# Kernel optimization log

Measured on AMD Instinct MI355X. Metric: run time of the kernel, lower is better.

The kernel has to match this reference:

```python
import jax, jax.numpy as jnp
import numpy as np

BETA = 0.25

def setup_inputs() -> dict:
    key = jax.random.key(0)
    k1, k2 = jax.random.split(key)
    N, K, D = 32768, 8192, 512
    latents = jax.random.normal(k1, (N, D), dtype=jnp.float32)
    # torch init: uniform(-1/num_protos, 1/num_protos)
    prototypes = jax.random.uniform(k2, (K, D), dtype=jnp.float32, minval=-1.0 / K, maxval=1.0 / K)
    return {"latents": latents, "prototypes": prototypes}


def reference(latents, prototypes):
    dists = (jnp.sum(latents ** 2, axis=1, keepdims=True)
             + jnp.sum(prototypes ** 2, axis=1)
             - 2.0 * jnp.matmul(latents, prototypes.T))
    closest = jnp.argmin(dists, axis=1)  # [N]
    # one-hot @ prototypes == gather (same math, no NxK intermediate)
    quantized = prototypes[closest]  # [N, D]
    commitment_loss = jnp.mean((jax.lax.stop_gradient(quantized) - latents) ** 2)
    embedding_loss = jnp.mean((quantized - jax.lax.stop_gradient(latents)) ** 2)
    vq_loss = commitment_loss * BETA + embedding_loss
    # straight-through estimator
    quantized_st = latents + jax.lax.stop_gradient(quantized - latents)
    return quantized_st, vq_loss
```

## Files before the change

### kernel.cpp

```cpp
#include <hip/hip_runtime.h>


#define N_ROWS 32768
#define K_PROTO 8192
#define DIM 512
#define BM 256
#define BN 128
#define BKB 128
#define GROUPS 8
#define TILES 8
#define NSTEP 32
#define BUFB 16384

typedef unsigned char u8;
typedef unsigned int u32;
typedef __attribute__((ext_vector_type(4))) int i32x4;
typedef __attribute__((ext_vector_type(8))) int i32x8;
typedef __attribute__((ext_vector_type(4))) float f32x4;

__device__ __forceinline__ void async16(const void* g, void* s) {
    __builtin_amdgcn_global_load_lds(
        (const __attribute__((address_space(1))) void*)g,
        (__attribute__((address_space(3))) void*)s, 16, 0, 0);
}

__device__ __forceinline__ int pk4(float a, float b, float c, float d) {
    int v = 0;
    v = __builtin_amdgcn_cvt_pk_fp8_f32(a, b, v, false);
    v = __builtin_amdgcn_cvt_pk_fp8_f32(c, d, v, true);
    return v;
}

__global__ void __launch_bounds__(256) conv_latents(const float* __restrict__ X,
                                                    u8* __restrict__ Xf,
                                                    u32* __restrict__ best) {
    if (blockIdx.x < 128) best[blockIdx.x * 256 + threadIdx.x] = 0xFFFFFFFFu;
    size_t i = ((size_t)blockIdx.x * 256 + threadIdx.x) * 16;
    float4 a = ((const float4*)(X + i))[0];
    float4 b = ((const float4*)(X + i))[1];
    float4 c = ((const float4*)(X + i))[2];
    float4 d = ((const float4*)(X + i))[3];
    int4 o;
    o.x = pk4(a.x, a.y, a.z, a.w);
    o.y = pk4(b.x, b.y, b.z, b.w);
    o.z = pk4(c.x, c.y, c.z, c.w);
    o.w = pk4(d.x, d.y, d.z, d.w);
    *(int4*)(Xf + i) = o;
}

__global__ void __launch_bounds__(256) conv_protos(const float* __restrict__ P,
                                                   u8* __restrict__ Pf,
                                                   float* __restrict__ pnC) {
    int row  = blockIdx.x * 4 + (threadIdx.x >> 6);
    int lane = threadIdx.x & 63;
    const float* src = P + (size_t)row * DIM + lane * 8;
    float4 a = ((const float4*)src)[0];
    float4 b = ((const float4*)src)[1];
    int2 o;
    o.x = pk4(a.x * 8192.0f, a.y * 8192.0f, a.z * 8192.0f, a.w * 8192.0f);
    o.y = pk4(b.x * 8192.0f, b.y * 8192.0f, b.z * 8192.0f, b.w * 8192.0f);
    *(int2*)(Pf + (size_t)row * DIM + lane * 8) = o;
    float ss = a.x*a.x + a.y*a.y + a.z*a.z + a.w*a.w
             + b.x*b.x + b.y*b.y + b.z*b.z + b.w*b.w;
    #pragma unroll
    for (int off = 32; off; off >>= 1) ss += __shfl_down(ss, off);
    if (lane == 0) pnC[row] = ss * 8192.0f + 256.0f;
}

__device__ __forceinline__ void stage_b(const u8* __restrict__ Pf, u8* BsF,
                                        int s2, int colg, const int (&voff)[4],
                                        int tid) {
    const int t2 = s2 >> 2, kt2 = s2 & 3, sb = s2 % 3;
    const u8* src = Pf + (size_t)(colg + t2 * BN) * DIM + kt2 * BKB;
    u8* dst = BsF + sb * BUFB + tid * 16;
    #pragma unroll
    for (int i = 0; i < 4; i++)
        async16(src + voff[i], dst + i * 4096);
}

__global__ void __launch_bounds__(256, 1) vq_score_kernel(const u8* __restrict__ Xf,
                                                          const u8* __restrict__ Pf,
                                                          const float* __restrict__ pnC,
                                                          u32* __restrict__ best) {
    __shared__ __align__(16) u8 lds_raw[3 * BUFB + 8192];
    u8* BsF = lds_raw;
    const float* pcs = (const float*)(lds_raw + 3 * BUFB);

    const int tid  = threadIdx.x;
    const int row0 = blockIdx.x * BM;
    const int colg = blockIdx.y * (TILES * BN);

    const int w    = tid >> 6, lane = tid & 63;
    const int quad = lane >> 4, l15 = lane & 15;

    int voff[4];
    #pragma unroll
    for (int i = 0; i < 4; i++) {
        int f = tid + i * 256;
        int row = f >> 3, c = (f & 7) ^ (row & 7);
        voff[i] = row * DIM + c * 16;
    }

    const int x7   = l15 & 7;
    const int pos0 = (quad ^ x7) << 4;
    const int pos1 = pos0 ^ 64;

    i32x8 a[4][4];
    {
        const u8* Ab = Xf + (size_t)(row0 + w * 64 + l15) * DIM + quad * 16;
        #pragma unroll
        for (int kt = 0; kt < 4; kt++)
            #pragma unroll
            for (int tm = 0; tm < 4; tm++) {
                const u8* p = Ab + (size_t)tm * 16 * DIM + kt * BKB;
                i32x4 lo = *(const i32x4*)p;
                i32x4 hi = *(const i32x4*)(p + 64);
                a[kt][tm] = __builtin_shufflevector(lo, hi, 0, 1, 2, 3, 4, 5, 6, 7);
            }
    }

    async16((const u8*)(pnC + colg) + tid * 16, lds_raw + 3 * BUFB + tid * 16);

    stage_b(Pf, BsF, 0, colg, voff, tid);
    stage_b(Pf, BsF, 1, colg, voff, tid);

    u32 v[4][4];
    #pragma unroll
    for (int i = 0; i < 4; i++)
        #pragma unroll
        for (int r = 0; r < 4; r++) v[i][r] = 0xFFFFFFFFu;

    for (int t = 0; t < TILES; ++t) {
        f32x4 acc[4][8];
        #pragma unroll
        for (int i = 0; i < 4; i++)
            #pragma unroll
            for (int j = 0; j < 8; j++) acc[i][j] = (f32x4)0.0f;

        #pragma unroll
        for (int kt = 0; kt < 4; ++kt) {
            const int s = t * 4 + kt;
            if (kt == 3 && t == TILES - 1)
                asm volatile("s_waitcnt vmcnt(0)" ::: "memory");
            else
                asm volatile("s_waitcnt vmcnt(4)" ::: "memory");
            __builtin_amdgcn_s_barrier();
            __builtin_amdgcn_sched_barrier(0);

            if (s + 2 < NSTEP) stage_b(Pf, BsF, s + 2, colg, voff, tid);

            const u8* Brow = BsF + (s % 3) * BUFB + l15 * BKB;
            __builtin_amdgcn_s_setprio(1);
            #pragma unroll
            for (int tn = 0; tn < 8; tn++) {
                const u8* bp = Brow + tn * 16 * BKB;
                i32x8 b = __builtin_shufflevector(
                    *(const i32x4*)(bp + pos0), *(const i32x4*)(bp + pos1),
                    0, 1, 2, 3, 4, 5, 6, 7);
                #pragma unroll
                for (int tm = 0; tm < 4; tm++)
                    acc[tm][tn] = __builtin_amdgcn_mfma_scale_f32_16x16x128_f8f6f4(
                        a[kt][tm], b, acc[tm][tn], 0, 0, 0, 127, 0, 127);
            }
            __builtin_amdgcn_s_setprio(0);
            __builtin_amdgcn_sched_barrier(0);
        }

        #pragma unroll
        for (int tn = 0; tn < 8; tn++) {
            const int ci = t * BN + tn * 16 + l15;
            const float pc = pcs[ci];
            const u32 kidx = (u32)(colg + ci);
            #pragma unroll
            for (int tm = 0; tm < 4; tm++)
                #pragma unroll
                for (int r = 0; r < 4; r++) {
                    float sk = fmaf(-2.0f, acc[tm][tn][r], pc);
                    u32 key = (__float_as_uint(sk) & 0xFFFFE000u) | kidx;
                    if (key < v[tm][r]) v[tm][r] = key;
                }
        }
    }

    #pragma unroll
    for (int tm = 0; tm < 4; tm++)
        #pragma unroll
        for (int r = 0; r < 4; r++) {
            u32 x = v[tm][r];
            #pragma unroll
            for (int off = 1; off < 16; off <<= 1) {
                u32 o = (u32)__shfl_xor((int)x, off);
                if (o < x) x = o;
            }
            if (l15 == 0)
                atomicMin(&best[row0 + w * 64 + tm * 16 + quad * 4 + r], x);
        }
}

__global__ void __launch_bounds__(128) vq_gather_kernel(const float* __restrict__ X,
                                                        const float* __restrict__ P,
                                                        const u32* __restrict__ best,
                                                        float* __restrict__ out,
                                                        float* __restrict__ partial) {
    const int n = blockIdx.x, t = threadIdx.x;
    const u32 k = best[n] & (K_PROTO - 1);
    const float4 p = ((const float4*)(P + (size_t)k * DIM))[t];
    const float4 x = ((const float4*)(X + (size_t)n * DIM))[t];
    ((float4*)(out + (size_t)n * DIM))[t] = p;
    float dx = p.x - x.x, dy = p.y - x.y, dz = p.z - x.z, dw = p.w - x.w;
    float ss = dx * dx + dy * dy + dz * dz + dw * dw;
    #pragma unroll
    for (int off = 32; off; off >>= 1) ss += __shfl_down(ss, off);
    __shared__ float part[2];
    if ((t & 63) == 0) part[t >> 6] = ss;
    __syncthreads();
    if (t == 0) partial[n] = part[0] + part[1];
}

__global__ void __launch_bounds__(256) loss_reduce(const float* __restrict__ partial,
                                                   float* __restrict__ out) {
    const int t = threadIdx.x;
    float s = 0.0f;
    #pragma unroll
    for (int i = 0; i < 32; i++) {
        float4 a = ((const float4*)partial)[t * 32 + i];
        s += a.x + a.y + a.z + a.w;
    }
    #pragma unroll
    for (int off = 32; off; off >>= 1) s += __shfl_down(s, off);
    __shared__ float part[4];
    if ((t & 63) == 0) part[t >> 6] = s;
    __syncthreads();
    if (t == 0)
        out[(size_t)N_ROWS * DIM] =
            (part[0] + part[1] + part[2] + part[3]) * 7.450580596923828e-08f;
}

extern "C" void kernel_launch(void* const* d_in, const int* in_sizes, int n_in,
                              void* d_out, int out_size, void* d_ws, size_t ws_size,
                              hipStream_t stream) {
    const float* X = (const float*)d_in[0];
    const float* P = (const float*)d_in[1];
    float* out = (float*)d_out;
    char* ws = (char*)d_ws;

    u8* Xf = (u8*)ws;
    u8* Pf = (u8*)(ws + 16777216);
    float* pnC = (float*)(ws + 20971520);
    u32* best = (u32*)(ws + 21004288);
    float* partial = (float*)(ws + 21135360);

    conv_latents<<<dim3(4096), dim3(256), 0, stream>>>(X, Xf, best);
    conv_protos<<<dim3(2048), dim3(256), 0, stream>>>(P, Pf, pnC);
    vq_score_kernel<<<dim3(N_ROWS / BM, GROUPS), dim3(256), 0, stream>>>(Xf, Pf, pnC, best);
    vq_gather_kernel<<<dim3(N_ROWS), dim3(128), 0, stream>>>(X, P, best, out, partial);
    loss_reduce<<<dim3(1), dim3(256), 0, stream>>>(partial, out);
}
```

Baseline: 313.8 us.

## Stream A and B tiles through LDS with 512-thread 4x2 warp layout

Replaces the register-resident A fragments (each warp holding its 64 rows across all of K) with double-buffered LDS staging of both the A and B tiles per K step. Blocks grow to 512 threads arranged as 4x2 warps, BN grows to 256, and each warp covers 64 rows by 128 prototype columns. The aim is to free the large register footprint held by the A fragments and to share the B tile across more warps. In exchange, A must be re-read from global and LDS on every step, and the pipeline drops from triple to double buffering.

```diff
diff --git a/kernel.cpp b/kernel.cpp
--- a/kernel.cpp
+++ b/kernel.cpp
@@ -5,12 +5,12 @@
 #define K_PROTO 8192
 #define DIM 512
 #define BM 256
-#define BN 128
+#define BN 256
 #define BKB 128
 #define GROUPS 8
-#define TILES 8
-#define NSTEP 32
-#define BUFB 16384
+#define TILES 4
+#define NSTEP 16
+#define HBUF 32768
 
 typedef unsigned char u8;
 typedef unsigned int u32;
@@ -67,36 +67,25 @@
     if (lane == 0) pnC[row] = ss * 8192.0f + 256.0f;
 }
 
-__device__ __forceinline__ void stage_b(const u8* __restrict__ Pf, u8* BsF,
-                                        int s2, int colg, const int (&voff)[4],
-                                        int tid) {
-    const int t2 = s2 >> 2, kt2 = s2 & 3, sb = s2 % 3;
-    const u8* src = Pf + (size_t)(colg + t2 * BN) * DIM + kt2 * BKB;
-    u8* dst = BsF + sb * BUFB + tid * 16;
-    #pragma unroll
-    for (int i = 0; i < 4; i++)
-        async16(src + voff[i], dst + i * 4096);
-}
-
-__global__ void __launch_bounds__(256, 1) vq_score_kernel(const u8* __restrict__ Xf,
+__global__ void __launch_bounds__(512, 1) vq_score_kernel(const u8* __restrict__ Xf,
                                                           const u8* __restrict__ Pf,
                                                           const float* __restrict__ pnC,
                                                           u32* __restrict__ best) {
-    __shared__ __align__(16) u8 lds_raw[3 * BUFB + 8192];
-    u8* BsF = lds_raw;
-    const float* pcs = (const float*)(lds_raw + 3 * BUFB);
+    __shared__ __align__(16) u8 lds_raw[4 * HBUF + 4096];
+    float* pcs = (float*)(lds_raw + 4 * HBUF);
 
     const int tid  = threadIdx.x;
     const int row0 = blockIdx.x * BM;
     const int colg = blockIdx.y * (TILES * BN);
 
     const int w    = tid >> 6, lane = tid & 63;
+    const int wm   = w >> 1,  wn   = w & 1;
     const int quad = lane >> 4, l15 = lane & 15;
 
     int voff[4];
     #pragma unroll
     for (int i = 0; i < 4; i++) {
-        int f = tid + i * 256;
+        int f = tid + i * 512;
         int row = f >> 3, c = (f & 7) ^ (row & 7);
         voff[i] = row * DIM + c * 16;
     }
@@ -105,24 +94,23 @@
     const int pos0 = (quad ^ x7) << 4;
     const int pos1 = pos0 ^ 64;
 
-    i32x8 a[4][4];
     {
-        const u8* Ab = Xf + (size_t)(row0 + w * 64 + l15) * DIM + quad * 16;
-        #pragma unroll
-        for (int kt = 0; kt < 4; kt++)
-            #pragma unroll
-            for (int tm = 0; tm < 4; tm++) {
-                const u8* p = Ab + (size_t)tm * 16 * DIM + kt * BKB;
-                i32x4 lo = *(const i32x4*)p;
-                i32x4 hi = *(const i32x4*)(p + 64);
-                a[kt][tm] = __builtin_shufflevector(lo, hi, 0, 1, 2, 3, 4, 5, 6, 7);
-            }
-    }
-
-    async16((const u8*)(pnC + colg) + tid * 16, lds_raw + 3 * BUFB + tid * 16);
-
-    stage_b(Pf, BsF, 0, colg, voff, tid);
-    stage_b(Pf, BsF, 1, colg, voff, tid);
+        const u8* As = Xf + (size_t)row0 * DIM;
+        const u8* Bsrc = Pf + (size_t)colg * DIM;
+        #pragma unroll
+        for (int i = 0; i < 4; i++) {
+            async16(As + voff[i], lds_raw + tid * 16 + i * 8192);
+            async16(Bsrc + voff[i], lds_raw + HBUF + tid * 16 + i * 8192);
+        }
+        if (tid < 256)
+            async16((const u8*)(pnC + colg) + tid * 16,
+                    lds_raw + 4 * HBUF + tid * 16);
+        #pragma unroll
+        for (int i = 0; i < 4; i++) {
+            async16(As + voff[i] + 1 * BKB, lds_raw + 2 * HBUF + tid * 16 + i * 8192);
+            async16(Bsrc + voff[i] + 1 * BKB, lds_raw + 3 * HBUF + tid * 16 + i * 8192);
+        }
+    }
 
     u32 v[4][4];
     #pragma unroll
@@ -140,27 +128,49 @@
         #pragma unroll
         for (int kt = 0; kt < 4; ++kt) {
             const int s = t * 4 + kt;
-            if (kt == 3 && t == TILES - 1)
+            __builtin_amdgcn_s_barrier();
+
+            if (s > 0 && s + 1 < NSTEP) {
+                const int s2 = s + 1;
+                const int kt2 = s2 & 3;
+                u8* dA = lds_raw + ((s2 & 1) ? 2 * HBUF : 0);
+                u8* dB = dA + HBUF;
+                const u8* As = Xf + (size_t)row0 * DIM + kt2 * BKB;
+                const u8* Bsrc = Pf + (size_t)(colg + (s2 >> 2) * BN) * DIM + kt2 * BKB;
+                #pragma unroll
+                for (int i = 0; i < 4; i++) {
+                    async16(As + voff[i], dA + tid * 16 + i * 8192);
+                    async16(Bsrc + voff[i], dB + tid * 16 + i * 8192);
+                }
+            }
+            if (s == NSTEP - 1)
                 asm volatile("s_waitcnt vmcnt(0)" ::: "memory");
             else
-                asm volatile("s_waitcnt vmcnt(4)" ::: "memory");
-            __builtin_amdgcn_s_barrier();
+                asm volatile("s_waitcnt vmcnt(8)" ::: "memory");
             __builtin_amdgcn_sched_barrier(0);
 
-            if (s + 2 < NSTEP) stage_b(Pf, BsF, s + 2, colg, voff, tid);
-
-            const u8* Brow = BsF + (s % 3) * BUFB + l15 * BKB;
+            const u8* Ab = lds_raw + ((s & 1) ? 2 * HBUF : 0);
+            const u8* Bb = Ab + HBUF;
+
+            i32x8 af[4];
+            #pragma unroll
+            for (int tm = 0; tm < 4; tm++) {
+                const u8* p = Ab + (wm * 64 + tm * 16 + l15) * BKB;
+                af[tm] = __builtin_shufflevector(*(const i32x4*)(p + pos0),
+                                                 *(const i32x4*)(p + pos1),
+                                                 0, 1, 2, 3, 4, 5, 6, 7);
+            }
             __builtin_amdgcn_s_setprio(1);
             #pragma unroll
             for (int tn = 0; tn < 8; tn++) {
-                const u8* bp = Brow + tn * 16 * BKB;
+                const u8* bp = Bb + (wn * 128 + tn * 16 + l15) * BKB;
                 i32x8 b = __builtin_shufflevector(
                     *(const i32x4*)(bp + pos0), *(const i32x4*)(bp + pos1),
                     0, 1, 2, 3, 4, 5, 6, 7);
                 #pragma unroll
                 for (int tm = 0; tm < 4; tm++)
                     acc[tm][tn] = __builtin_amdgcn_mfma_scale_f32_16x16x128_f8f6f4(
-                        a[kt][tm], b, acc[tm][tn], 0, 0, 0, 127, 0, 127);
+                        af[tm], b, acc[tm][tn], 0, 0, 0, 127, 0, 127);
             }
             __builtin_amdgcn_s_setprio(0);
             __builtin_amdgcn_sched_barrier(0);
@@ -168,7 +178,7 @@
 
         #pragma unroll
         for (int tn = 0; tn < 8; tn++) {
-            const int ci = t * BN + tn * 16 + l15;
+            const int ci = t * BN + wn * 128 + tn * 16 + l15;
             const float pc = pcs[ci];
             const u32 kidx = (u32)(colg + ci);
             #pragma unroll
@@ -193,7 +203,7 @@
                 if (o < x) x = o;
             }
             if (l15 == 0)
-                atomicMin(&best[row0 + w * 64 + tm * 16 + quad * 4 + r], x);
+                atomicMin(&best[row0 + wm * 64 + tm * 16 + quad * 4 + r], x);
         }
 }
 
@@ -252,7 +262,7 @@
 
     conv_latents<<<dim3(4096), dim3(256), 0, stream>>>(X, Xf, best);
     conv_protos<<<dim3(2048), dim3(256), 0, stream>>>(P, Pf, pnC);
-    vq_score_kernel<<<dim3(N_ROWS / BM, GROUPS), dim3(256), 0, stream>>>(Xf, Pf, pnC, best);
+    vq_score_kernel<<<dim3(N_ROWS / BM, GROUPS), dim3(512), 0, stream>>>(Xf, Pf, pnC, best);
     vq_gather_kernel<<<dim3(N_ROWS), dim3(128), 0, stream>>>(X, P, best, out, partial);
     loss_reduce<<<dim3(1), dim3(256), 0, stream>>>(partial, out);
 }
```

Measured after the change: 883.8 us. +181.6%, slower.
